# Kernel optimization log

Hardware: AMD Instinct MI355X
Metric: run time of the kernel (lower is better)

Reference implementation:

```python
import jax, jax.numpy as jnp
import numpy as np


def setup_inputs() -> dict:
    key = jax.random.key(0)
    k1, k2 = jax.random.split(key)
    B, D, H, W = 32, 256, 32, 32
    K = 1024
    z = jax.random.normal(k1, (B, D, H, W), dtype=jnp.float32)
    # torch init is uniform(-1/K, 1/K); randn scaled keeps same scale class
    embedding_weight = jax.random.uniform(k2, (K, D), dtype=jnp.float32,
                                          minval=-1.0 / K, maxval=1.0 / K)
    return {"z": z, "embedding_weight": embedding_weight}


def reference(z, embedding_weight):
    # z: [B, D, H, W] -> [B, H, W, D]
    z_nhwc = jnp.transpose(z, (0, 2, 3, 1))
    B, H, W, D = z_nhwc.shape
    z_flat = z_nhwc.reshape(-1, D)                      # [N, D]
    # squared distances: ||z||^2 + ||e||^2 - 2 z @ e^T   -> [N, K]
    d = (jnp.sum(z_flat ** 2, axis=1, keepdims=True)
         + jnp.sum(embedding_weight ** 2, axis=1)
         - 2.0 * z_flat @ embedding_weight.T)
    min_encoding_indices = jnp.argmin(d, axis=1)        # [N] int
    z_q = embedding_weight[min_encoding_indices].reshape(B, H, W, D)
    memodecode_loss = (jax.lax.stop_gradient(z_q) - z_nhwc) ** 2  # [B,H,W,D]
    z_q_out = jnp.transpose(z_q, (0, 3, 1, 2))          # [B, D, H, W]
    return (z_q_out, min_encoding_indices, memodecode_loss)
```

## Files before the change

### kernel.cpp

```cpp
#include <hip/hip_runtime.h>

#define DD 256
#define HWN 1024
#define NN 32768
#define KK 1024
#define MARGIN 1e-4f
#define FLAGBIT (1 << 30)

#define ZQ_OFF   0
#define IDX_OFF  8388608
#define LOSS_OFF 8421376

#define WS_NEED 38146112

typedef __attribute__((ext_vector_type(8))) _Float16 f16x8;
typedef __attribute__((ext_vector_type(4))) float f32x4;
typedef unsigned long long u64;

__device__ __forceinline__ ushort f2h(float x) {
    _Float16 h = (_Float16)x;
    return *reinterpret_cast<ushort*>(&h);
}
__device__ __forceinline__ float h2f(ushort u) {
    _Float16 h = *reinterpret_cast<_Float16*>(&u);
    return (float)h;
}

__device__ __forceinline__ int swz(int r, int kgi) {
    return (r << 2) + (kgi ^ (r & 3) ^ ((r >> 2) & 3));
}

__global__ __launch_bounds__(256) void k_e2(const float* __restrict__ E,
                                            float* __restrict__ e2) {
    const int th = threadIdx.x;
    const int row = (blockIdx.x << 5) + (th >> 3);
    const int j = th & 7;
    const float* a = E + (size_t)row * DD;
    float x0 = a[j];
    float r0 = __fmul_rn(x0, x0);
    float x1 = a[128 + j];
    float r1 = __fmul_rn(x1, x1);
#pragma unroll
    for (int i = 8; i < 128; i += 8) {
        float y0 = a[i + j];
        r0 = __fadd_rn(r0, __fmul_rn(y0, y0));
        float y1 = a[128 + i + j];
        r1 = __fadd_rn(r1, __fmul_rn(y1, y1));
    }
#pragma unroll
    for (int m = 1; m <= 4; m <<= 1) {
        r0 = __fadd_rn(r0, __shfl_xor(r0, m));
        r1 = __fadd_rn(r1, __shfl_xor(r1, m));
    }
    if (j == 0) e2[row] = __fadd_rn(r0, r1);
}

__global__ __launch_bounds__(256) void k_prepZ2(const float* __restrict__ Z,
                                                ushort* __restrict__ Zh,
                                                float* __restrict__ z2) {
    __shared__ float zc[32][257];
    const int g = blockIdx.x;
    const int b = g >> 5;
    const int hw0 = (g & 31) << 5;
    const int th = threadIdx.x;
    const int n0 = (b << 10) + hw0;

#pragma unroll
    for (int j = 0; j < 32; ++j) {
        int li = (j << 8) + th;
        int d = li >> 5;
        int hl = li & 31;
        zc[hl][d] = Z[(size_t)((b << 8) + d) * HWN + hw0 + hl];
    }
    __syncthreads();

    {
        int r = th >> 3, c = th & 7;
        ushort hs[32];
#pragma unroll
        for (int i = 0; i < 32; ++i) hs[i] = f2h(zc[r][(c << 5) + i]);
        size_t addr = (size_t)(n0 + r) * DD + (c << 5);
#pragma unroll
        for (int q = 0; q < 4; ++q)
            *reinterpret_cast<f16x8*>(&Zh[addr + (q << 3)]) =
                *reinterpret_cast<f16x8*>(&hs[q << 3]);
    }

    {
        const int row = th >> 3, j = th & 7;
        const float* a = &zc[row][0];
        float x0 = a[j];
        float r0 = __fmul_rn(x0, x0);
        float x1 = a[128 + j];
        float r1 = __fmul_rn(x1, x1);
#pragma unroll
        for (int i = 8; i < 128; i += 8) {
            float y0 = a[i + j];
            r0 = __fadd_rn(r0, __fmul_rn(y0, y0));
            float y1 = a[128 + i + j];
            r1 = __fadd_rn(r1, __fmul_rn(y1, y1));
        }
#pragma unroll
        for (int m = 1; m <= 4; m <<= 1) {
            r0 = __fadd_rn(r0, __shfl_xor(r0, m));
            r1 = __fadd_rn(r1, __shfl_xor(r1, m));
        }
        if (j == 0) z2[n0 + row] = __fadd_rn(r0, r1);
    }
}

__global__ __launch_bounds__(256) void k_z2(const float* __restrict__ Z,
                                            float* __restrict__ z2) {
    int n = (blockIdx.x << 8) + threadIdx.x;
    int b = n >> 10, hw = n & 1023;
    const float* base = Z + (size_t)(b << 8) * HWN + hw;
    float half_[2];
#pragma unroll
    for (int h = 0; h < 2; ++h) {
        const float* a = base + (size_t)(h << 7) * HWN;
        float r[8];
#pragma unroll
        for (int j = 0; j < 8; ++j) {
            float x = a[(size_t)j * HWN];
            r[j] = __fmul_rn(x, x);
        }
        for (int i = 8; i < 128; i += 8) {
#pragma unroll
            for (int j = 0; j < 8; ++j) {
                float x = a[(size_t)(i + j) * HWN];
                r[j] = __fadd_rn(r[j], __fmul_rn(x, x));
            }
        }
        half_[h] = __fadd_rn(__fadd_rn(__fadd_rn(r[0], r[1]), __fadd_rn(r[2], r[3])),
                             __fadd_rn(__fadd_rn(r[4], r[5]), __fadd_rn(r[6], r[7])));
    }
    z2[n] = __fadd_rn(half_[0], half_[1]);
}

__global__ __launch_bounds__(256) void k_prepE(const float* __restrict__ E,
                                               ushort* __restrict__ Eh,
                                               int* __restrict__ flagCount) {
    if (blockIdx.x == 0 && threadIdx.x == 0) *flagCount = 0;
    int i4 = (blockIdx.x << 8) + threadIdx.x;
    float4 v = *reinterpret_cast<const float4*>(&E[(size_t)i4 << 2]);
    v.x *= 1024.f; v.y *= 1024.f; v.z *= 1024.f; v.w *= 1024.f;
    ushort4 h;
    h.x = f2h(v.x); h.y = f2h(v.y); h.z = f2h(v.z); h.w = f2h(v.w);
    *reinterpret_cast<ushort4*>(&Eh[(size_t)i4 << 2]) = h;
}

__device__ __forceinline__ void stage_kc(const ushort* __restrict__ Zh,
                                         const ushort* __restrict__ Eh,
                                         ushort* ldsbuf, int n0, int c0, int kc,
                                         int wid, int lane) {
#pragma unroll
    for (int is = 0; is < 4; ++is) {
        const int chunk = (wid << 2) + is;
        const int arr = chunk >> 3;
        const int cb8 = chunk & 7;
        const int s = (cb8 << 6) + lane;
        const int r = s >> 2;
        const int kgi = (s & 3) ^ (r & 3) ^ ((r >> 2) & 3);
        const ushort* g = (arr == 0) ? Zh + (size_t)(n0 + r) * DD
                                     : Eh + (size_t)(c0 + r) * DD;
        g += (kc << 5) + (kgi << 3);
        ushort* l = ldsbuf + arr * 4096 + (cb8 << 9);
        __builtin_amdgcn_global_load_lds(
            (const __attribute__((address_space(1))) void*)g,
            (__attribute__((address_space(3))) void*)l, 16, 0, 0);
    }
}

__global__ __launch_bounds__(256) void k_dist_mfma(const ushort* __restrict__ Zh,
                                                   const ushort* __restrict__ Eh,
                                                   const float* __restrict__ e2,
                                                   float* __restrict__ part) {
    __shared__ ushort lds[2][2][4096];
    float (*red)[2][3] = reinterpret_cast<float (*)[2][3]>(&lds[0][0][0]);

    const int B = blockIdx.x;
    const int xcd = B & 7;
    const int j = B >> 3;
    const int cb = j & 7;
    const int rb = (xcd << 5) + (j >> 3);
    const int n0 = rb << 7, c0 = cb << 7;
    const int th = threadIdx.x;
    const int wid = th >> 6, lane = th & 63;
    const int wr = wid >> 1, wc = wid & 1;
    const int fr = lane & 15, kgi = lane >> 4;

    f32x4 acc[4][4];
#pragma unroll
    for (int i = 0; i < 4; ++i)
#pragma unroll
        for (int jj = 0; jj < 4; ++jj) acc[i][jj] = (f32x4){0.f, 0.f, 0.f, 0.f};

    int zoff[4], eoff[4];
#pragma unroll
    for (int mi = 0; mi < 4; ++mi)
        zoff[mi] = swz((wr << 6) + (mi << 4) + fr, kgi) << 4;
#pragma unroll
    for (int ni = 0; ni < 4; ++ni)
        eoff[ni] = swz((wc << 6) + (ni << 4) + fr, kgi) << 4;

    stage_kc(Zh, Eh, &lds[0][0][0], n0, c0, 0, wid, lane);

    for (int kc = 0; kc < 8; ++kc) {
        __builtin_amdgcn_s_barrier();
        if (kc < 7) {
            stage_kc(Zh, Eh, &lds[(kc + 1) & 1][0][0], n0, c0, kc + 1, wid, lane);
            asm volatile("s_waitcnt vmcnt(4)" ::: "memory");
        } else {
            asm volatile("s_waitcnt vmcnt(0)" ::: "memory");
        }
        __builtin_amdgcn_s_barrier();

        const char* zb  = (const char*)&lds[kc & 1][0][0];
        const char* ebh = (const char*)&lds[kc & 1][1][0];
        f16x8 za[4], ea[4];
#pragma unroll
        for (int mi = 0; mi < 4; ++mi)
            za[mi] = *reinterpret_cast<const f16x8*>(zb + zoff[mi]);
#pragma unroll
        for (int ni = 0; ni < 4; ++ni)
            ea[ni] = *reinterpret_cast<const f16x8*>(ebh + eoff[ni]);
        __builtin_amdgcn_s_setprio(1);
#pragma unroll
        for (int mi = 0; mi < 4; ++mi)
#pragma unroll
            for (int ni = 0; ni < 4; ++ni)
                acc[mi][ni] = __builtin_amdgcn_mfma_f32_16x16x32_f16(za[mi], ea[ni], acc[mi][ni], 0, 0, 0);
        __builtin_amdgcn_s_setprio(0);
    }

    __syncthreads();

    float e2v[4];
#pragma unroll
    for (int ni = 0; ni < 4; ++ni) e2v[ni] = e2[c0 + (wc << 6) + (ni << 4) + fr];

#pragma unroll
    for (int mi = 0; mi < 4; ++mi) {
#pragma unroll
        for (int jj = 0; jj < 4; ++jj) {
            float m1 = __builtin_inff(), m2 = __builtin_inff(), bi = 3.4e38f;
#pragma unroll
            for (int ni = 0; ni < 4; ++ni) {
                float s = fmaf(-0x1p-9f, acc[mi][ni][jj], e2v[ni]);
                float c = (float)(c0 + (wc << 6) + (ni << 4) + fr);
                if (s < m1)      { m2 = m1; m1 = s; bi = c; }
                else if (s < m2) { m2 = s; }
            }
#pragma unroll
            for (int m = 1; m <= 8; m <<= 1) {
                float om1 = __shfl_xor(m1, m);
                float om2 = __shfl_xor(m2, m);
                float obi = __shfl_xor(bi, m);
                if (om1 < m1)       { m2 = fminf(m1, om2); m1 = om1; bi = obi; }
                else if (om1 == m1) { bi = fminf(bi, obi); m2 = m1; }
                else                { m2 = fminf(m2, om1); }
            }
            if (fr == 0) {
                int row = (wr << 6) + (mi << 4) + (kgi << 2) + jj;
                red[row][wc][0] = m1; red[row][wc][1] = m2; red[row][wc][2] = bi;
            }
        }
    }
    __syncthreads();
    if (th < 128) {
        float M1 = red[th][0][0], M2 = red[th][0][1], I = red[th][0][2];
        float v1 = red[th][1][0], v2 = red[th][1][1], vi = red[th][1][2];
        if (v1 < M1)       { M2 = fminf(M1, v2); M1 = v1; I = vi; }
        else if (v1 == M1) { I = fminf(I, vi); M2 = M1; }
        else               { M2 = fminf(M2, v1); }
        size_t p = ((size_t)(n0 + th) * 8 + cb) * 3;
        part[p] = M1; part[p + 1] = M2; part[p + 2] = I;
    }
}

__global__ __launch_bounds__(256) void k_combine(const float* __restrict__ part,
                                                 int* __restrict__ bestIdx,
                                                 int* __restrict__ flagList,
                                                 int* __restrict__ flagCount,
                                                 u64* __restrict__ bestG) {
    int n = (blockIdx.x << 8) + threadIdx.x;
    const float* p = part + (size_t)n * 24;
    float M1 = __builtin_inff(), M2 = __builtin_inff(), I = 3.4e38f;
    for (int c = 0; c < 8; ++c) {
        float v1 = p[c * 3], v2 = p[c * 3 + 1], vi = p[c * 3 + 2];
        if (v1 < M1)       { M2 = fminf(M1, v2); M1 = v1; I = vi; }
        else if (v1 == M1) { I = fminf(I, vi); M2 = M1; }
        else               { M2 = fminf(M2, v1); }
    }
    bestIdx[n] = (int)I;
    if (M2 - M1 < MARGIN) {
        bestG[n] = ~0ull;
        int pos = atomicAdd(flagCount, 1);
        flagList[pos] = n;
    }
}

__global__ __launch_bounds__(256) void k_refine5(const float* __restrict__ Z,
                                                 const float* __restrict__ E,
                                                 const float* __restrict__ e2,
                                                 const float* __restrict__ z2,
                                                 const int* __restrict__ flagList,
                                                 const int* __restrict__ flagCount,
                                                 u64* __restrict__ bestG) {
    __shared__ float zsh[4][DD];
    __shared__ float gbv[16][4];
    __shared__ int gbi[16][4];
    __shared__ int rown[4];
    const int th = threadIdx.x;
    const int g = th >> 4;
    const int l = th & 15;
    const int cnt = *flagCount;
    const int items = ((cnt + 3) >> 2) << 2;

    for (int jj = blockIdx.x; jj < items; jj += (int)gridDim.x) {
        const int gi = jj >> 2;
        const int q = jj & 3;
        __syncthreads();
        if (th < 4) {
            int fi = (gi << 2) + th;
            if (fi >= cnt) fi = cnt - 1;
            rown[th] = flagList[fi];
        }
        __syncthreads();
#pragma unroll
        for (int r = 0; r < 4; ++r) {
            int n = rown[r];
            zsh[r][th] = Z[(size_t)(((n >> 10) << 8) + th) * HWN + (n & 1023)];
        }
        __syncthreads();
        float zr[4][16];
#pragma unroll
        for (int r = 0; r < 4; ++r)
#pragma unroll
            for (int jq = 0; jq < 16; ++jq) zr[r][jq] = zsh[r][(l << 4) + jq];
        float z2v[4];
#pragma unroll
        for (int r = 0; r < 4; ++r) z2v[r] = z2[rown[r]];
        float gbest[4];
        int bi[4];
#pragma unroll
        for (int r = 0; r < 4; ++r) { gbest[r] = __builtin_inff(); bi[r] = 0; }

        const int base = q << 8;
        for (int it = 0; it < 4; ++it) {
#pragma unroll
            for (int u = 0; u < 4; ++u) {
                const int c = base + (it << 6) + (u << 4) + g;
                const float* er = &E[(size_t)c * DD + (l << 4)];
                float4 a0 = *reinterpret_cast<const float4*>(er);
                float4 a1 = *reinterpret_cast<const float4*>(er + 4);
                float4 a2 = *reinterpret_cast<const float4*>(er + 8);
                float4 a3 = *reinterpret_cast<const float4*>(er + 12);
                double dots[4];
#pragma unroll
                for (int r = 0; r < 4; ++r) {
                    double s0 = (double)a0.x * zr[r][0]  + (double)a0.y * zr[r][1]
                              + (double)a0.z * zr[r][2]  + (double)a0.w * zr[r][3];
                    double s1 = (double)a1.x * zr[r][4]  + (double)a1.y * zr[r][5]
                              + (double)a1.z * zr[r][6]  + (double)a1.w * zr[r][7];
                    double s2 = (double)a2.x * zr[r][8]  + (double)a2.y * zr[r][9]
                              + (double)a2.z * zr[r][10] + (double)a2.w * zr[r][11];
                    double s3 = (double)a3.x * zr[r][12] + (double)a3.y * zr[r][13]
                              + (double)a3.z * zr[r][14] + (double)a3.w * zr[r][15];
                    dots[r] = (s0 + s1) + (s2 + s3);
                }
#pragma unroll
                for (int m = 1; m <= 8; m <<= 1) {
#pragma unroll
                    for (int r = 0; r < 4; ++r)
                        dots[r] += __shfl_xor(dots[r], m);
                }
                if (l == 0) {
#pragma unroll
                    for (int r = 0; r < 4; ++r) {
                        float cc = (float)dots[r];
                        float t2 = __fmul_rn(2.0f, cc);
                        float gg = __fsub_rn(__fadd_rn(z2v[r], e2[c]), t2);
                        if (gg < gbest[r]) { gbest[r] = gg; bi[r] = c; }
                    }
                }
            }
        }
        if (l == 0) {
#pragma unroll
            for (int r = 0; r < 4; ++r) { gbv[g][r] = gbest[r]; gbi[g][r] = bi[r]; }
        }
        __syncthreads();
        if (th < 4) {
            const int r = th;
            float best = gbv[0][r]; int bbi = gbi[0][r];
            for (int qq = 1; qq < 16; ++qq) {
                float v = gbv[qq][r]; int vi = gbi[qq][r];
                if (v < best || (v == best && vi < bbi)) { best = v; bbi = vi; }
            }
            u64 pack = ((u64)__float_as_uint(best) << 32) | (unsigned)bbi;
            atomicMin(&bestG[rown[r]], pack);
        }
    }
}

__global__ __launch_bounds__(256) void k_final(const int* __restrict__ flagList,
                                               const int* __restrict__ flagCount,
                                               const u64* __restrict__ bestG,
                                               int* __restrict__ bestIdx) {
    const int cnt = *flagCount;
    for (int j = (blockIdx.x << 8) + threadIdx.x; j < cnt; j += (int)(gridDim.x << 8)) {
        int n = flagList[j];
        bestIdx[n] = (int)(unsigned)(bestG[n] & 0xFFFFFFFFull);
    }
}

#define UPD(m1, m2, i1, s, k)                            \
    do {                                                 \
        if ((s) < (m1)) { m2 = m1; m1 = (s); i1 = (k); } \
        else if ((s) < (m2)) { m2 = (s); }               \
    } while (0)

#define FMAJ(j, EV, C)                                   \
    acc[0][j] = fmaf(z4.x, EV.C, acc[0][j]);             \
    acc[1][j] = fmaf(z4.y, EV.C, acc[1][j]);             \
    acc[2][j] = fmaf(z4.z, EV.C, acc[2][j]);             \
    acc[3][j] = fmaf(z4.w, EV.C, acc[3][j]);

#define UROUND(u, C)                                                          \
    {                                                                         \
        float4 z4 = *reinterpret_cast<const float4*>(&zs[dq + u][ty4]);       \
        FMAJ(0, e0, C) FMAJ(1, e1, C) FMAJ(2, e2v, C) FMAJ(3, e3, C)          \
        FMAJ(4, e4, C) FMAJ(5, e5, C) FMAJ(6, e6, C) FMAJ(7, e7, C)           \
    }

__global__ __launch_bounds__(256, 3) void k_dist_f32(const float* __restrict__ Z,
                                                     const float* __restrict__ E,
                                                     const float* __restrict__ e2,
                                                     int* __restrict__ bestIdx) {
    __shared__ float zs[64][68];
    __shared__ float es[128][68];
    const int th = threadIdx.x;
    const int n0 = blockIdx.x << 6;
    const int b = n0 >> 10;
    const int hw0 = n0 & 1023;
    const int tx = th & 15;
    const int ty = th >> 4;
    const int ty4 = ty << 2;
    float m1[4], m2[4];
    int idx[4];
#pragma unroll
    for (int i = 0; i < 4; ++i) { m1[i] = __builtin_inff(); m2[i] = __builtin_inff(); idx[i] = 0; }
    for (int ct = 0; ct < 8; ++ct) {
        float acc[4][8];
#pragma unroll
        for (int i = 0; i < 4; ++i)
#pragma unroll
            for (int j = 0; j < 8; ++j) acc[i][j] = 0.f;
        for (int dc = 0; dc < 4; ++dc) {
            __syncthreads();
#pragma unroll
            for (int j = 0; j < 4; ++j) {
                int i4 = (j << 8) + th;
                int dd = i4 >> 4;
                int rr = (i4 & 15) << 2;
                *reinterpret_cast<float4*>(&zs[dd][rr]) =
                    *reinterpret_cast<const float4*>(
                        &Z[(size_t)((b << 8) + (dc << 6) + dd) * HWN + hw0 + rr]);
            }
#pragma unroll
            for (int j = 0; j < 8; ++j) {
                int i4 = (j << 8) + th;
                int c = i4 >> 4;
                int d4 = (i4 & 15) << 2;
                *reinterpret_cast<float4*>(&es[c][d4]) =
                    *reinterpret_cast<const float4*>(
                        &E[(size_t)((ct << 7) + c) * DD + (dc << 6) + d4]);
            }
            __syncthreads();
#pragma unroll
            for (int dq = 0; dq < 64; dq += 4) {
                float4 e0 = *reinterpret_cast<const float4*>(&es[tx][dq]);
                float4 e1 = *reinterpret_cast<const float4*>(&es[tx + 16][dq]);
                float4 e2v = *reinterpret_cast<const float4*>(&es[tx + 32][dq]);
                float4 e3 = *reinterpret_cast<const float4*>(&es[tx + 48][dq]);
                float4 e4 = *reinterpret_cast<const float4*>(&es[tx + 64][dq]);
                float4 e5 = *reinterpret_cast<const float4*>(&es[tx + 80][dq]);
                float4 e6 = *reinterpret_cast<const float4*>(&es[tx + 96][dq]);
                float4 e7 = *reinterpret_cast<const float4*>(&es[tx + 112][dq]);
                UROUND(0, x)
                UROUND(1, y)
                UROUND(2, z)
                UROUND(3, w)
            }
        }
#pragma unroll
        for (int j = 0; j < 8; ++j) {
            int c = (ct << 7) + tx + (j << 4);
            float en = e2[c];
#pragma unroll
            for (int i = 0; i < 4; ++i) {
                float s = fmaf(-2.f, acc[i][j], en);
                UPD(m1[i], m2[i], idx[i], s, c);
            }
        }
    }
    __syncthreads();
    float* red = &es[0][0];
#pragma unroll
    for (int i = 0; i < 4; ++i) {
        int r = ty4 + i;
        int base = ((r << 4) + tx) * 3;
        red[base] = m1[i]; red[base + 1] = m2[i]; red[base + 2] = (float)idx[i];
    }
    __syncthreads();
    if (th < 64) {
        float M1 = __builtin_inff(), M2 = __builtin_inff(), I = 3.4e38f;
        for (int t = 0; t < 16; ++t) {
            int base = ((th << 4) + t) * 3;
            float v1 = red[base], v2 = red[base + 1], vi = red[base + 2];
            if (v1 < M1)       { M2 = fminf(M1, v2); M1 = v1; I = vi; }
            else if (v1 == M1) { I = fminf(I, vi); M2 = fminf(M2, v1); M2 = fminf(M2, v2); }
            else               { M2 = fminf(M2, v1); }
        }
        int id = (int)I;
        bestIdx[n0 + th] = (M2 - M1 < MARGIN) ? (id | FLAGBIT) : id;
    }
}

__global__ __launch_bounds__(64) void k_refine(const float* __restrict__ Z,
                                               const float* __restrict__ E,
                                               const float* __restrict__ e2,
                                               const float* __restrict__ z2,
                                               int* __restrict__ bestIdx) {
    __shared__ float zr[DD];
    const int l = threadIdx.x;
    for (int i = 0; i < 16; ++i) {
        int n = (blockIdx.x << 4) + i;
        if (!(bestIdx[n] & FLAGBIT)) continue;
        int b = n >> 10, hw = n & 1023;
        __syncthreads();
#pragma unroll
        for (int j = 0; j < 4; ++j)
            zr[(l << 2) + j] = Z[(size_t)((b << 8) + (l << 2) + j) * HWN + hw];
        __syncthreads();
        const float z2v = z2[n];
        float gbest = __builtin_inff();
        int bi = KK;
        for (int kk = 0; kk < 16; ++kk) {
            int k = (kk << 6) + l;
            double dot = 0.0;
            for (int d = 0; d < DD; d += 4) {
                float4 e4 = *reinterpret_cast<const float4*>(&E[(size_t)k * DD + d]);
                dot += (double)e4.x * zr[d]     + (double)e4.y * zr[d + 1]
                     + (double)e4.z * zr[d + 2] + (double)e4.w * zr[d + 3];
            }
            float c = (float)dot;
            float t = __fmul_rn(2.0f, c);
            float gg = __fsub_rn(__fadd_rn(z2v, e2[k]), t);
            if (gg < gbest) { gbest = gg; bi = k; }
        }
#pragma unroll
        for (int off = 32; off > 0; off >>= 1) {
            float og = __shfl_down(gbest, off);
            int oi = __shfl_down(bi, off);
            if (og < gbest || (og == gbest && oi < bi)) { gbest = og; bi = oi; }
        }
        if (l == 0) bestIdx[n] = bi;
    }
}

__global__ __launch_bounds__(256) void k_out(const ushort* __restrict__ Zh,
                                             const float* __restrict__ E,
                                             const int* __restrict__ bestIdx,
                                             float* __restrict__ out) {
    __shared__ int idxs[64];
    __shared__ float es[64][68];
    const int th = threadIdx.x;
    const int n0 = blockIdx.x << 6;
    const int b = n0 >> 10;
    const int hw0 = n0 & 1023;

    if (th < 64) {
        int id = bestIdx[n0 + th] & 1023;
        idxs[th] = id;
        out[IDX_OFF + n0 + th] = (float)id;
    }
    __syncthreads();

#pragma unroll
    for (int j = 0; j < 16; ++j) {
        int i4 = (j << 8) + th;
        int r = i4 >> 6;
        int f = (i4 & 63) << 2;
        int n = n0 + r;
        float4 e4 = *reinterpret_cast<const float4*>(&E[(size_t)idxs[r] * DD + f]);
        ushort4 zu = *reinterpret_cast<const ushort4*>(&Zh[(size_t)n * DD + f]);
        float4 o;
        float t;
        t = e4.x - h2f(zu.x); o.x = t * t;
        t = e4.y - h2f(zu.y); o.y = t * t;
        t = e4.z - h2f(zu.z); o.z = t * t;
        t = e4.w - h2f(zu.w); o.w = t * t;
        *reinterpret_cast<float4*>(&out[LOSS_OFF + (size_t)n * DD + f]) = o;
    }

    for (int dc = 0; dc < 4; ++dc) {
        __syncthreads();
        {
            const int r = th >> 2, qd = (th & 3) << 4;
            const float* er = &E[(size_t)idxs[r] * DD + (dc << 6) + qd];
#pragma unroll
            for (int v = 0; v < 4; ++v)
                *reinterpret_cast<float4*>(&es[r][qd + (v << 2)]) =
                    *reinterpret_cast<const float4*>(er + (v << 2));
        }
        __syncthreads();
#pragma unroll
        for (int j = 0; j < 16; ++j) {
            int li = (j << 8) + th;
            int dd = li >> 6;
            int r = li & 63;
            out[ZQ_OFF + (size_t)((b << 8) + (dc << 6) + dd) * HWN + hw0 + r] =
                es[r][dd];
        }
    }
}

__global__ __launch_bounds__(256) void k_out_f32(const float* __restrict__ Z,
                                                 const float* __restrict__ E,
                                                 const int* __restrict__ bestIdx,
                                                 float* __restrict__ out) {
    __shared__ float zc[64][68];
    __shared__ int idxs[64];
    const int th = threadIdx.x;
    const int n0 = blockIdx.x << 6;
    const int b = n0 >> 10;
    const int hw0 = n0 & 1023;

    if (th < 64) {
        int id = bestIdx[n0 + th] & 1023;
        idxs[th] = id;
        out[IDX_OFF + n0 + th] = (float)id;
    }
    __syncthreads();

    for (int dc = 0; dc < 4; ++dc) {
        __syncthreads();
#pragma unroll
        for (int j = 0; j < 16; ++j) {
            int li = (j << 8) + th;
            int dd = li >> 6;
            int r = li & 63;
            zc[r][dd] = Z[(size_t)((b << 8) + (dc << 6) + dd) * HWN + hw0 + r];
        }
        __syncthreads();
#pragma unroll
        for (int j = 0; j < 4; ++j) {
            int i4 = (j << 8) + th;
            int r = i4 >> 4;
            int f = (i4 & 15) << 2;
            float4 e4 = *reinterpret_cast<const float4*>(
                &E[(size_t)idxs[r] * DD + (dc << 6) + f]);
            float4 z4 = *reinterpret_cast<const float4*>(&zc[r][f]);
            float4 o;
            o.x = (e4.x - z4.x) * (e4.x - z4.x);
            o.y = (e4.y - z4.y) * (e4.y - z4.y);
            o.z = (e4.z - z4.z) * (e4.z - z4.z);
            o.w = (e4.w - z4.w) * (e4.w - z4.w);
            *reinterpret_cast<float4*>(
                &out[LOSS_OFF + (size_t)(n0 + r) * DD + (dc << 6) + f]) = o;
        }
#pragma unroll
        for (int j = 0; j < 16; ++j) {
            int li = (j << 8) + th;
            int dd = li >> 6;
            int r = li & 63;
            out[ZQ_OFF + (size_t)((b << 8) + (dc << 6) + dd) * HWN + hw0 + r] =
                E[(size_t)idxs[r] * DD + (dc << 6) + dd];
        }
    }
}

extern "C" void kernel_launch(void* const* d_in, const int* in_sizes, int n_in,
                              void* d_out, int out_size, void* d_ws, size_t ws_size,
                              hipStream_t stream) {
    const float* Z = (const float*)d_in[0];
    const float* E = (const float*)d_in[1];
    float* out = (float*)d_out;
    char* ws = (char*)d_ws;
    float* e2 = (float*)ws;
    float* z2 = (float*)(ws + 4096);
    int* bestIdx = (int*)(ws + 135168);

    k_e2<<<32, 256, 0, stream>>>(E, e2);

    if (ws_size >= WS_NEED) {
        float* part = (float*)(ws + 266240);
        ushort* Eh = (ushort*)(ws + 3411968);
        ushort* Zh = (ushort*)(ws + 4460544);
        u64* bestG = (u64*)(ws + 21237760);
        int* flagCount = (int*)(ws + 38014976);
        int* flagList = (int*)(ws + 38015040);
        k_prepE<<<256, 256, 0, stream>>>(E, Eh, flagCount);
        k_prepZ2<<<1024, 256, 0, stream>>>(Z, Zh, z2);
        k_dist_mfma<<<2048, 256, 0, stream>>>(Zh, Eh, e2, part);
        k_combine<<<NN / 256, 256, 0, stream>>>(part, bestIdx, flagList, flagCount, bestG);
        k_refine5<<<2048, 256, 0, stream>>>(Z, E, e2, z2, flagList, flagCount, bestG);
        k_final<<<64, 256, 0, stream>>>(flagList, flagCount, bestG, bestIdx);
        k_out<<<NN / 64, 256, 0, stream>>>(Zh, E, bestIdx, out);
    } else {
        k_z2<<<NN / 256, 256, 0, stream>>>(Z, z2);
        k_dist_f32<<<NN / 64, 256, 0, stream>>>(Z, E, e2, bestIdx);
        k_refine<<<NN / 16, 64, 0, stream>>>(Z, E, e2, z2, bestIdx);
        k_out_f32<<<NN / 64, 256, 0, stream>>>(Z, E, bestIdx, out);
    }
}
```

Before: 137.7 us.

## Pre-tile and swizzle fp16 operands, fuse prep kernels, drop final fixup kernel

The prep kernels now write Z and E in fp16 into a tiled, pre-swizzled layout that matches the MFMA LDS staging, so each global_load_lds reads contiguous 16-byte chunks per lane with no per-load swizzle arithmetic. The E squared norms and fp16 conversion are fused into one kernel, and the k_final fixup kernel is removed by flagging refined rows in bestIdx and resolving them in k_out from bestG. This removes two launches and improves load coalescing, at the cost of an extra Zh2 copy written during prep (more write traffic and workspace).

```diff
diff --git a/kernel.cpp b/kernel.cpp
--- a/kernel.cpp
+++ b/kernel.cpp
@@ -30,33 +30,59 @@
     return (r << 2) + (kgi ^ (r & 3) ^ ((r >> 2) & 3));
 }
 
-__global__ __launch_bounds__(256) void k_e2(const float* __restrict__ E,
-                                            float* __restrict__ e2) {
+__global__ __launch_bounds__(256) void k_prepE2(const float* __restrict__ E,
+                                                ushort* __restrict__ Eh2,
+                                                float* __restrict__ e2,
+                                                int* __restrict__ flagCount) {
+    __shared__ float ec[32][257];
+    const int g = blockIdx.x;
     const int th = threadIdx.x;
-    const int row = (blockIdx.x << 5) + (th >> 3);
-    const int j = th & 7;
-    const float* a = E + (size_t)row * DD;
-    float x0 = a[j];
-    float r0 = __fmul_rn(x0, x0);
-    float x1 = a[128 + j];
-    float r1 = __fmul_rn(x1, x1);
-#pragma unroll
-    for (int i = 8; i < 128; i += 8) {
-        float y0 = a[i + j];
-        r0 = __fadd_rn(r0, __fmul_rn(y0, y0));
-        float y1 = a[128 + i + j];
-        r1 = __fadd_rn(r1, __fmul_rn(y1, y1));
-    }
-#pragma unroll
-    for (int m = 1; m <= 4; m <<= 1) {
-        r0 = __fadd_rn(r0, __shfl_xor(r0, m));
-        r1 = __fadd_rn(r1, __shfl_xor(r1, m));
-    }
-    if (j == 0) e2[row] = __fadd_rn(r0, r1);
+    const int n0 = g << 5;
+    if (g == 0 && th == 0) *flagCount = 0;
+#pragma unroll
+    for (int j = 0; j < 32; ++j)
+        ec[j][th] = E[(size_t)n0 * DD + (j << 8) + th];
+    __syncthreads();
+    {
+        const int r = th & 31, c = th >> 5;
+        const int row = n0 + r;
+        const int t = row >> 7, rl = row & 127;
+        ushort hs[32];
+#pragma unroll
+        for (int i = 0; i < 32; ++i)
+            hs[i] = f2h(__fmul_rn(ec[r][(c << 5) + i], 1024.f));
+        ushort* sb = Eh2 + (size_t)c * 32768 + (size_t)t * 4096;
+#pragma unroll
+        for (int kgi = 0; kgi < 4; ++kgi)
+            *reinterpret_cast<f16x8*>(&sb[swz(rl, kgi) << 3]) =
+                *reinterpret_cast<f16x8*>(&hs[kgi << 3]);
+    }
+    {
+        const int row = th >> 3, j = th & 7;
+        const float* a = &ec[row][0];
+        float x0 = a[j];
+        float r0 = __fmul_rn(x0, x0);
+        float x1 = a[128 + j];
+        float r1 = __fmul_rn(x1, x1);
+#pragma unroll
+        for (int i = 8; i < 128; i += 8) {
+            float y0 = a[i + j];
+            r0 = __fadd_rn(r0, __fmul_rn(y0, y0));
+            float y1 = a[128 + i + j];
+            r1 = __fadd_rn(r1, __fmul_rn(y1, y1));
+        }
+#pragma unroll
+        for (int m = 1; m <= 4; m <<= 1) {
+            r0 = __fadd_rn(r0, __shfl_xor(r0, m));
+            r1 = __fadd_rn(r1, __shfl_xor(r1, m));
+        }
+        if (j == 0) e2[n0 + row] = __fadd_rn(r0, r1);
+    }
 }
 
 __global__ __launch_bounds__(256) void k_prepZ2(const float* __restrict__ Z,
                                                 ushort* __restrict__ Zh,
+                                                ushort* __restrict__ Zh2,
                                                 float* __restrict__ z2) {
     __shared__ float zc[32][257];
     const int g = blockIdx.x;
@@ -75,15 +101,22 @@
     __syncthreads();
 
     {
-        int r = th >> 3, c = th & 7;
+        const int r = th & 31, c = th >> 5;
+        const int n = n0 + r;
+        const int t = n >> 7, rl = n & 127;
         ushort hs[32];
 #pragma unroll
         for (int i = 0; i < 32; ++i) hs[i] = f2h(zc[r][(c << 5) + i]);
-        size_t addr = (size_t)(n0 + r) * DD + (c << 5);
+        size_t addr = (size_t)n * DD + (c << 5);
 #pragma unroll
         for (int q = 0; q < 4; ++q)
             *reinterpret_cast<f16x8*>(&Zh[addr + (q << 3)]) =
                 *reinterpret_cast<f16x8*>(&hs[q << 3]);
+        ushort* sb = Zh2 + (size_t)c * 1048576 + (size_t)t * 4096;
+#pragma unroll
+        for (int kgi = 0; kgi < 4; ++kgi)
+            *reinterpret_cast<f16x8*>(&sb[swz(rl, kgi) << 3]) =
+                *reinterpret_cast<f16x8*>(&hs[kgi << 3]);
     }
 
     {
@@ -137,33 +170,18 @@
     z2[n] = __fadd_rn(half_[0], half_[1]);
 }
 
-__global__ __launch_bounds__(256) void k_prepE(const float* __restrict__ E,
-                                               ushort* __restrict__ Eh,
-                                               int* __restrict__ flagCount) {
-    if (blockIdx.x == 0 && threadIdx.x == 0) *flagCount = 0;
-    int i4 = (blockIdx.x << 8) + threadIdx.x;
-    float4 v = *reinterpret_cast<const float4*>(&E[(size_t)i4 << 2]);
-    v.x *= 1024.f; v.y *= 1024.f; v.z *= 1024.f; v.w *= 1024.f;
-    ushort4 h;
-    h.x = f2h(v.x); h.y = f2h(v.y); h.z = f2h(v.z); h.w = f2h(v.w);
-    *reinterpret_cast<ushort4*>(&Eh[(size_t)i4 << 2]) = h;
-}
-
-__device__ __forceinline__ void stage_kc(const ushort* __restrict__ Zh,
-                                         const ushort* __restrict__ Eh,
-                                         ushort* ldsbuf, int n0, int c0, int kc,
+__device__ __forceinline__ void stage_kc(const ushort* __restrict__ Zs,
+                                         const ushort* __restrict__ Es,
+                                         ushort* ldsbuf, int zt, int et, int kc,
                                          int wid, int lane) {
 #pragma unroll
     for (int is = 0; is < 4; ++is) {
         const int chunk = (wid << 2) + is;
         const int arr = chunk >> 3;
         const int cb8 = chunk & 7;
-        const int s = (cb8 << 6) + lane;
-        const int r = s >> 2;
-        const int kgi = (s & 3) ^ (r & 3) ^ ((r >> 2) & 3);
-        const ushort* g = (arr == 0) ? Zh + (size_t)(n0 + r) * DD
-                                     : Eh + (size_t)(c0 + r) * DD;
-        g += (kc << 5) + (kgi << 3);
+        const ushort* g = (arr == 0)
+            ? Zs + (size_t)kc * 1048576 + (size_t)zt * 4096 + (cb8 << 9) + (lane << 3)
+            : Es + (size_t)kc * 32768  + (size_t)et * 4096 + (cb8 << 9) + (lane << 3);
         ushort* l = ldsbuf + arr * 4096 + (cb8 << 9);
         __builtin_amdgcn_global_load_lds(
             (const __attribute__((address_space(1))) void*)g,
@@ -171,8 +189,8 @@
     }
 }
 
-__global__ __launch_bounds__(256) void k_dist_mfma(const ushort* __restrict__ Zh,
-                                                   const ushort* __restrict__ Eh,
+__global__ __launch_bounds__(256) void k_dist_mfma(const ushort* __restrict__ Zh2,
+                                                   const ushort* __restrict__ Eh2,
                                                    const float* __restrict__ e2,
                                                    float* __restrict__ part) {
     __shared__ ushort lds[2][2][4096];
@@ -203,12 +221,12 @@
     for (int ni = 0; ni < 4; ++ni)
         eoff[ni] = swz((wc << 6) + (ni << 4) + fr, kgi) << 4;
 
-    stage_kc(Zh, Eh, &lds[0][0][0], n0, c0, 0, wid, lane);
+    stage_kc(Zh2, Eh2, &lds[0][0][0], rb, cb, 0, wid, lane);
 
     for (int kc = 0; kc < 8; ++kc) {
         __builtin_amdgcn_s_barrier();
         if (kc < 7) {
-            stage_kc(Zh, Eh, &lds[(kc + 1) & 1][0][0], n0, c0, kc + 1, wid, lane);
+            stage_kc(Zh2, Eh2, &lds[(kc + 1) & 1][0][0], rb, cb, kc + 1, wid, lane);
             asm volatile("s_waitcnt vmcnt(4)" ::: "memory");
         } else {
             asm volatile("s_waitcnt vmcnt(0)" ::: "memory");
@@ -292,11 +310,13 @@
         else if (v1 == M1) { I = fminf(I, vi); M2 = M1; }
         else               { M2 = fminf(M2, v1); }
     }
-    bestIdx[n] = (int)I;
     if (M2 - M1 < MARGIN) {
+        bestIdx[n] = (int)I | FLAGBIT;
         bestG[n] = ~0ull;
         int pos = atomicAdd(flagCount, 1);
         flagList[pos] = n;
+    } else {
+        bestIdx[n] = (int)I;
     }
 }
 
@@ -404,17 +424,6 @@
     }
 }
 
-__global__ __launch_bounds__(256) void k_final(const int* __restrict__ flagList,
-                                               const int* __restrict__ flagCount,
-                                               const u64* __restrict__ bestG,
-                                               int* __restrict__ bestIdx) {
-    const int cnt = *flagCount;
-    for (int j = (blockIdx.x << 8) + threadIdx.x; j < cnt; j += (int)(gridDim.x << 8)) {
-        int n = flagList[j];
-        bestIdx[n] = (int)(unsigned)(bestG[n] & 0xFFFFFFFFull);
-    }
-}
-
 #define UPD(m1, m2, i1, s, k)                            \
     do {                                                 \
         if ((s) < (m1)) { m2 = m1; m1 = (s); i1 = (k); } \
@@ -573,6 +582,7 @@
 __global__ __launch_bounds__(256) void k_out(const ushort* __restrict__ Zh,
                                              const float* __restrict__ E,
                                              const int* __restrict__ bestIdx,
+                                             const u64* __restrict__ bestG,
                                              float* __restrict__ out) {
     __shared__ int idxs[64];
     __shared__ float es[64][68];
@@ -582,9 +592,11 @@
     const int hw0 = n0 & 1023;
 
     if (th < 64) {
-        int id = bestIdx[n0 + th] & 1023;
+        int n = n0 + th;
+        int v = bestIdx[n];
+        int id = (v & FLAGBIT) ? (int)(unsigned)(bestG[n] & 1023ull) : (v & 1023);
         idxs[th] = id;
-        out[IDX_OFF + n0 + th] = (float)id;
+        out[IDX_OFF + n] = (float)id;
     }
     __syncthreads();
 
@@ -693,24 +705,23 @@
     float* z2 = (float*)(ws + 4096);
     int* bestIdx = (int*)(ws + 135168);
 
-    k_e2<<<32, 256, 0, stream>>>(E, e2);
-
     if (ws_size >= WS_NEED) {
         float* part = (float*)(ws + 266240);
-        ushort* Eh = (ushort*)(ws + 3411968);
-        ushort* Zh = (ushort*)(ws + 4460544);
-        u64* bestG = (u64*)(ws + 21237760);
-        int* flagCount = (int*)(ws + 38014976);
-        int* flagList = (int*)(ws + 38015040);
-        k_prepE<<<256, 256, 0, stream>>>(E, Eh, flagCount);
-        k_prepZ2<<<1024, 256, 0, stream>>>(Z, Zh, z2);
-        k_dist_mfma<<<2048, 256, 0, stream>>>(Zh, Eh, e2, part);
+        ushort* Eh2 = (ushort*)(ws + 3411968);
+        ushort* Zh = (ushort*)(ws + 3936256);
+        ushort* Zh2 = (ushort*)(ws + 20713472);
+        u64* bestG = (u64*)(ws + 37490688);
+        int* flagCount = (int*)(ws + 37752832);
+        int* flagList = (int*)(ws + 37752896);
+        k_prepE2<<<32, 256, 0, stream>>>(E, Eh2, e2, flagCount);
+        k_prepZ2<<<1024, 256, 0, stream>>>(Z, Zh, Zh2, z2);
+        k_dist_mfma<<<2048, 256, 0, stream>>>(Zh2, Eh2, e2, part);
         k_combine<<<NN / 256, 256, 0, stream>>>(part, bestIdx, flagList, flagCount, bestG);
         k_refine5<<<2048, 256, 0, stream>>>(Z, E, e2, z2, flagList, flagCount, bestG);
-        k_final<<<64, 256, 0, stream>>>(flagList, flagCount, bestG, bestIdx);
-        k_out<<<NN / 64, 256, 0, stream>>>(Zh, E, bestIdx, out);
+        k_out<<<NN / 64, 256, 0, stream>>>(Zh, E, bestIdx, bestG, out);
     } else {
         k_z2<<<NN / 256, 256, 0, stream>>>(Z, z2);
+        k_prepE2<<<32, 256, 0, stream>>>(E, (ushort*)(ws + 266240), e2, (int*)(ws + 266240 + 524288));
         k_dist_f32<<<NN / 64, 256, 0, stream>>>(Z, E, e2, bestIdx);
         k_refine<<<NN / 16, 64, 0, stream>>>(Z, E, e2, z2, bestIdx);
         k_out_f32<<<NN / 64, 256, 0, stream>>>(Z, E, bestIdx, out);
```

After: 143.3 us. +4.1%, slower.
